# Kernel optimization log

Measured on AMD Instinct MI355X. Metric: run time of the kernel, lower is better.

The kernel has to match this reference:

```python
import jax, jax.numpy as jnp
import numpy as np
import math

N_HEAD = 12

def alibi_slopes(h):
    x = (2 ** 8) ** (1.0 / h)
    return jnp.array([1.0 / x ** (i + 1) for i in range(h)], dtype=jnp.float32)

def setup_inputs() -> dict:
    key = jax.random.key(0)
    k0, k1, k2 = jax.random.split(key, 3)
    B, T, C = 4, 2048, 576
    x = jax.random.normal(k0, (B, T, C), dtype=jnp.float32)
    w_qkv = jax.random.normal(k1, (3 * C, C), dtype=jnp.float32) * 0.02
    w_proj = jax.random.normal(k2, (C, C), dtype=jnp.float32) * 0.02
    return {"x": x, "w_qkv": w_qkv, "w_proj": w_proj}

def reference(x, w_qkv, w_proj):
    B, T, C = x.shape
    H = N_HEAD
    D = C // H
    qkv = x @ w_qkv.T  # [B,T,3C]
    q, k, v = jnp.split(qkv, 3, axis=2)
    q = q.reshape(B, T, H, D).transpose(0, 2, 1, 3)  # [B,H,T,D]
    k = k.reshape(B, T, H, D).transpose(0, 2, 1, 3)
    v = v.reshape(B, T, H, D).transpose(0, 2, 1, 3)
    # value residual with v1=None: v = 0.5*v + 0.5*v = v (faithful no-op)
    scale = 1.0 / math.sqrt(D)
    att = jnp.einsum('bhid,bhjd->bhij', q, k) * scale  # [B,H,T,T]
    # ALiBi bias as written: (col - row).clamp(min=0) * slope (zero on causal part)
    col = jnp.arange(T, dtype=jnp.float32)[None, :]
    row = jnp.arange(T, dtype=jnp.float32)[:, None]
    bias = jnp.maximum(col - row, 0.0)[None, :, :] * alibi_slopes(H)[:, None, None]  # [H,T,T]
    att = att + bias[None]
    causal = (jnp.arange(T)[None, :] <= jnp.arange(T)[:, None])  # [T,T] lower-tri
    att = jnp.where(causal[None, None], att, -jnp.inf)
    att = jax.nn.softmax(att, axis=-1)
    y = jnp.einsum('bhij,bhjd->bhid', att, v)  # [B,H,T,D]
    y = y.transpose(0, 2, 1, 3).reshape(B, T, C)
    return y @ w_proj.T
```

## Files before the change

### kernel.cpp

```cpp
#include <hip/hip_runtime.h>
#include <math.h>

#define Bn 4
#define Tn 2048
#define Cn 576
#define Hn 12
#define Dn 48
#define Mn (Bn*Tn)

#define QSCALE (1.4426950408889634f * 0.14433756729740643f)

typedef short  short8  __attribute__((ext_vector_type(8)));
typedef float  floatx4 __attribute__((ext_vector_type(4)));
typedef unsigned short ushort_t;
typedef unsigned short ushort8_t __attribute__((ext_vector_type(8)));

static __device__ __forceinline__ unsigned short f2bf(float f) {
    union { float f; unsigned int u; } v; v.f = f;
    unsigned int r = v.u + 0x7FFFu + ((v.u >> 16) & 1u);
    return (unsigned short)(r >> 16);
}

static __device__ __forceinline__ unsigned int pack_trunc(float a, float b) {
    union { float f; unsigned int u; } ua, ub; ua.f = a; ub.f = b;
    return (ua.u >> 16) | (ub.u & 0xFFFF0000u);
}

static __device__ __forceinline__ void gload16(void* lds, const void* g) {
    __builtin_amdgcn_global_load_lds(
        (const __attribute__((address_space(1))) void*)g,
        (__attribute__((address_space(3))) void*)lds, 16, 0, 0);
}

__global__ __launch_bounds__(256)
void cast3(const float* __restrict__ a, ushort_t* __restrict__ oa, int na4,
           const float* __restrict__ b, ushort_t* __restrict__ ob, int nb4,
           const float* __restrict__ c, ushort_t* __restrict__ oc, int nc4)
{
    int i = blockIdx.x * 256 + threadIdx.x;
    const float* src; ushort_t* dst; int idx;
    if (i < na4)                  { src = a; dst = oa; idx = i; }
    else if (i < na4 + nb4)       { src = b; dst = ob; idx = i - na4; }
    else if (i < na4 + nb4 + nc4) { src = c; dst = oc; idx = i - na4 - nb4; }
    else return;
    float4 v = ((const float4*)src)[idx];
    ushort4 o;
    o.x = f2bf(v.x); o.y = f2bf(v.y); o.z = f2bf(v.z); o.w = f2bf(v.w);
    ((ushort4*)dst)[idx] = o;
}

template<int MODE, int MTILE>
__global__ __launch_bounds__(256)
void gemm_mfma(const ushort_t* __restrict__ A, const ushort_t* __restrict__ W,
               ushort_t* __restrict__ outb, float* __restrict__ outf)
{
    constexpr int SA   = MTILE / 16;
    constexpr int NSEG = SA + 4;
    constexpr int PW   = NSEG / 4;
    constexpr int MF   = MTILE / 64;
    constexpr int NB   = (MODE == 0) ? 27 : 9;
    __shared__ __align__(16) ushort_t Ls[2][NSEG][512];

    const int tid  = threadIdx.x;
    const int wave = tid >> 6;
    const int lane = tid & 63;
    const int m    = lane & 15;
    const int g    = lane >> 4;
    const int bid  = blockIdx.x;
    const int xcd  = bid & 7;
    const int slot = bid >> 3;
    const int n0   = (slot % NB) * 64;
    const int m0   = (xcd + 8 * (slot / NB)) * MTILE;

    floatx4 acc[MF][4];
    #pragma unroll
    for (int i = 0; i < MF; ++i)
        #pragma unroll
        for (int j = 0; j < 4; ++j)
            acc[i][j] = (floatx4){0.f, 0.f, 0.f, 0.f};

    const char* gp[PW];
    int         si[PW];
    #pragma unroll
    for (int i = 0; i < PW; ++i) {
        int s = wave + i * 4;
        si[i] = s;
        gp[i] = (s < SA)
            ? (const char*)(A + (size_t)(m0 + s * 16 + m) * Cn + g * 8)
            : (const char*)(W + (size_t)(n0 + (s - SA) * 16 + m) * Cn + g * 8);
    }

    #pragma unroll
    for (int i = 0; i < PW; ++i) { gload16(&Ls[0][si[i]][0], gp[i]); gp[i] += 64; }
    __syncthreads();

    int buf = 0;
    for (int k0 = 0; k0 < Cn; k0 += 32) {
        if (k0 + 32 < Cn) {
            #pragma unroll
            for (int i = 0; i < PW; ++i) { gload16(&Ls[buf ^ 1][si[i]][0], gp[i]); gp[i] += 64; }
        }
        short8 bf4[4];
        #pragma unroll
        for (int j = 0; j < 4; ++j) bf4[j] = *(const short8*)&Ls[buf][SA + j][lane * 8];
        #pragma unroll
        for (int i = 0; i < MF; ++i) {
            short8 af = *(const short8*)&Ls[buf][wave * MF + i][lane * 8];
            #pragma unroll
            for (int j = 0; j < 4; ++j)
                acc[i][j] = __builtin_amdgcn_mfma_f32_16x16x32_bf16(af, bf4[j], acc[i][j], 0, 0, 0);
        }
        __syncthreads();
        buf ^= 1;
    }

    const size_t per = (size_t)Bn * Hn * Tn * Dn;
    if (MODE == 0) {
        const int which = n0 / Cn;
        const int nb    = n0 - which * Cn;
        const int b     = m0 >> 11;
        const int t0g   = m0 & 2047;
        ushort_t* Lc = (ushort_t*)&Ls[0][0][0];
        if (which == 2) {
            constexpr int RS = MTILE + 8;
            #pragma unroll
            for (int i = 0; i < MF; ++i)
                #pragma unroll
                for (int j = 0; j < 4; ++j) {
                    ushort4 pk;
                    pk.x = f2bf(acc[i][j][0]); pk.y = f2bf(acc[i][j][1]);
                    pk.z = f2bf(acc[i][j][2]); pk.w = f2bf(acc[i][j][3]);
                    *(ushort4*)&Lc[(j * 16 + m) * RS + wave * (MTILE / 4) + i * 16 + g * 4] = pk;
                }
            __syncthreads();
            constexpr int CPC = MTILE / 8;
            constexpr int NIT = 64 * CPC / 256;
            #pragma unroll
            for (int it = 0; it < NIT; ++it) {
                int c    = tid + it * 256;
                int col  = c / CPC;
                int rowc = (c - col * CPC) * 8;
                int n    = nb + col;
                int h    = n / 48;
                int d    = n - h * 48;
                ushort_t* dst = outb + 2 * per
                    + (((size_t)(b * Hn + h) * Dn + d) * Tn) + t0g + rowc;
                *(ushort8_t*)dst = *(const ushort8_t*)&Lc[col * RS + rowc];
            }
        } else {
            const float sc = (which == 0) ? QSCALE : 1.0f;
            #pragma unroll
            for (int i = 0; i < MF; ++i)
                #pragma unroll
                for (int j = 0; j < 4; ++j)
                    #pragma unroll
                    for (int r = 0; r < 4; ++r)
                        Lc[(wave * (MTILE / 4) + i * 16 + g * 4 + r) * 80 + j * 16 + m] =
                            f2bf(acc[i][j][r] * sc);
            __syncthreads();
            constexpr int NIT = MTILE * 8 / 256;
            #pragma unroll
            for (int it = 0; it < NIT; ++it) {
                int c   = tid + it * 256;
                int row = c >> 3;
                int c8  = (c & 7) * 8;
                int n   = nb + c8;
                int h   = n / 48;
                int d   = n - h * 48;
                ushort_t* dst = outb + (size_t)which * per
                    + (((size_t)(b * Hn + h) * Tn + t0g + row) * Dn) + d;
                *(ushort8_t*)dst = *(const ushort8_t*)&Lc[row * 80 + c8];
            }
        }
    } else {
        #pragma unroll
        for (int i = 0; i < MF; ++i) {
            #pragma unroll
            for (int r = 0; r < 4; ++r) {
                int mrow = m0 + wave * (MTILE / 4) + i * 16 + g * 4 + r;
                #pragma unroll
                for (int j = 0; j < 4; ++j)
                    outf[(size_t)mrow * Cn + n0 + j * 16 + m] = acc[i][j][r];
            }
        }
    }
}

__global__ __launch_bounds__(512, 6)
void attn_mfma(const ushort_t* __restrict__ Q, const ushort_t* __restrict__ K,
               const ushort_t* __restrict__ V, ushort_t* __restrict__ Y,
               const ushort_t* __restrict__ zb)
{
    __shared__ __align__(16) ushort_t QPs[16][512];
    __shared__ __align__(16) ushort_t Ks[2][8][512];
    __shared__ __align__(16) ushort_t Vs[2][6][512];

    const int id   = blockIdx.x;
    const int kk   = id / 48;
    const int bh   = id - kk * 48;
    const int QT   = (kk & 1) ? (kk >> 1) : (15 - (kk >> 1));
    const int tid  = threadIdx.x;
    const int wave = tid >> 6;
    const int lane = tid & 63;
    const int m    = lane & 15;
    const int g    = lane >> 4;
    const int q0   = QT * 128;
    const int nkt  = 2 * QT + 2;

    const ushort_t* Qp = Q + (size_t)bh * Tn * Dn;
    const ushort_t* Kp = K + (size_t)bh * Tn * Dn;
    const ushort_t* Vp = V + (size_t)bh * Dn * Tn;

    {
        const char* qrp = (const char*)(Qp + (size_t)(q0 + wave * 16 + m) * Dn);
        gload16(&QPs[wave * 2 + 0][0], qrp + g * 16);
        gload16(&QPs[wave * 2 + 1][0], (g < 2) ? (qrp + 64 + g * 16) : (const char*)zb);
    }

    const bool  kpad = ((wave & 1) == 1) && (g >= 2);
    const char* kptr = kpad ? (const char*)zb
        : (const char*)(Kp + (size_t)((wave >> 1) * 16 + m) * Dn) + (wave & 1) * 64 + g * 16;
    const int   kadv = kpad ? 0 : 64 * Dn * 2;
    const char* vptr = (const char*)(Vp + (size_t)((wave >> 1) * 16 + m) * Tn)
                       + (wave & 1) * 64 + g * 16;
    const int   vadv = 64 * 2;

    gload16(&Ks[0][wave][0], kptr); kptr += kadv;
    if (wave < 6) { gload16(&Vs[0][wave][0], vptr); vptr += vadv; }
    __syncthreads();

    short8 bq[2];
    bq[0] = *(const short8*)&QPs[wave * 2 + 0][lane * 8];
    bq[1] = *(const short8*)&QPs[wave * 2 + 1][lane * 8];

    floatx4 acc[3];
    #pragma unroll
    for (int t = 0; t < 3; ++t) acc[t] = (floatx4){0.f, 0.f, 0.f, 0.f};
    float l_tot = 0.f;
    const int qrow  = q0 + wave * 16 + m;
    const int qwmin = q0 + wave * 16;
    const int qwmax = qwmin + 15;

    for (int jt = 0; jt < nkt; ++jt) {
        const int cur = jt & 1;
        const int j0  = jt * 64;
        if (jt + 1 < nkt) {
            gload16(&Ks[cur ^ 1][wave][0], kptr); kptr += kadv;
            if (wave < 6) { gload16(&Vs[cur ^ 1][wave][0], vptr); vptr += vadv; }
        }

        if (j0 <= qwmax) {
            floatx4 s[4];
            #pragma unroll
            for (int t = 0; t < 4; ++t) {
                s[t] = (floatx4){0.f, 0.f, 0.f, 0.f};
                #pragma unroll
                for (int kc = 0; kc < 2; ++kc) {
                    short8 ak = *(const short8*)&Ks[cur][t * 2 + kc][lane * 8];
                    s[t] = __builtin_amdgcn_mfma_f32_16x16x32_bf16(ak, bq[kc], s[t], 0, 0, 0);
                }
            }

            float p[4][4];
            float lsum = 0.f;
            if (j0 + 63 > qwmin) {
                #pragma unroll
                for (int t = 0; t < 4; ++t)
                    #pragma unroll
                    for (int r = 0; r < 4; ++r) {
                        int j = j0 + t * 16 + g * 4 + r;
                        float v = (j <= qrow) ? s[t][r] : -1e30f;
                        float e = __builtin_amdgcn_exp2f(v);
                        p[t][r] = e; lsum += e;
                    }
            } else {
                #pragma unroll
                for (int t = 0; t < 4; ++t)
                    #pragma unroll
                    for (int r = 0; r < 4; ++r) {
                        float e = __builtin_amdgcn_exp2f(s[t][r]);
                        p[t][r] = e; lsum += e;
                    }
            }
            lsum += __shfl_xor(lsum, 16);
            lsum += __shfl_xor(lsum, 32);
            l_tot += lsum;

            #pragma unroll
            for (int t = 0; t < 4; ++t) {
                uint2 w2;
                w2.x = pack_trunc(p[t][0], p[t][1]);
                w2.y = pack_trunc(p[t][2], p[t][3]);
                *(uint2*)&QPs[wave * 2 + (t >> 1)]
                             [(2 * (t & 1) + (g >> 1)) * 128 + m * 8 + (g & 1) * 4] = w2;
            }
            asm volatile("s_waitcnt lgkmcnt(0)" ::: "memory");

            #pragma unroll
            for (int kc = 0; kc < 2; ++kc) {
                short8 bp = *(const short8*)&QPs[wave * 2 + kc][lane * 8];
                #pragma unroll
                for (int t = 0; t < 3; ++t) {
                    short8 av = *(const short8*)&Vs[cur][t * 2 + kc][lane * 8];
                    acc[t] = __builtin_amdgcn_mfma_f32_16x16x32_bf16(av, bp, acc[t], 0, 0, 0);
                }
            }
        }

        __syncthreads();
    }

    const float inv = 1.0f / l_tot;
    const int b = bh / Hn;
    const int h = bh - b * Hn;
    ushort_t* yp = Y + ((size_t)(b * Tn + qrow)) * Cn + h * Dn;
    #pragma unroll
    for (int t = 0; t < 3; ++t) {
        ushort4 o;
        o.x = f2bf(acc[t][0] * inv);
        o.y = f2bf(acc[t][1] * inv);
        o.z = f2bf(acc[t][2] * inv);
        o.w = f2bf(acc[t][3] * inv);
        *(ushort4*)&yp[t * 16 + g * 4] = o;
    }
}

extern "C" void kernel_launch(void* const* d_in, const int* in_sizes, int n_in,
                              void* d_out, int out_size, void* d_ws, size_t ws_size,
                              hipStream_t stream)
{
    const float* x      = (const float*)d_in[0];
    const float* w_qkv  = (const float*)d_in[1];
    const float* w_proj = (const float*)d_in[2];
    float* out = (float*)d_out;

    const size_t per = (size_t)Bn * Hn * Tn * Dn;

    ushort_t* xb  = (ushort_t*)d_ws;
    ushort_t* wqb = xb  + (size_t)Mn * Cn;
    ushort_t* wpb = wqb + (size_t)3 * Cn * Cn;
    ushort_t* qkv = wpb + (size_t)Cn * Cn;
    ushort_t* yb  = qkv + 3 * per;
    ushort_t* zb  = yb  + (size_t)Mn * Cn;

    hipMemsetAsync(zb, 0, 256, stream);

    const int na4 = Mn * Cn / 4, nb4 = 3 * Cn * Cn / 4, nc4 = Cn * Cn / 4;
    cast3<<<dim3((na4 + nb4 + nc4 + 255) / 256), dim3(256), 0, stream>>>(
        x, xb, na4, w_qkv, wqb, nb4, w_proj, wpb, nc4);

    gemm_mfma<0, 256><<<dim3((Mn / 256) * 27), dim3(256), 0, stream>>>(xb, wqb, qkv, nullptr);

    attn_mfma<<<dim3((Tn / 128) * Bn * Hn), dim3(512), 0, stream>>>(
        qkv, qkv + per, qkv + 2 * per, yb, zb);

    gemm_mfma<1, 128><<<dim3((Mn / 128) * 9), dim3(256), 0, stream>>>(yb, wpb, nullptr, out);
}
```

Baseline: 186.5 us.

## Load GEMM operands directly into registers instead of staging through LDS

```diff
diff --git a/kernel.cpp b/kernel.cpp
--- a/kernel.cpp
+++ b/kernel.cpp
@@ -49,17 +49,14 @@
     ((ushort4*)dst)[idx] = o;
 }
 
-template<int MODE, int MTILE>
-__global__ __launch_bounds__(256)
+template<int MODE>
+__global__ __launch_bounds__(256, 2)
 void gemm_mfma(const ushort_t* __restrict__ A, const ushort_t* __restrict__ W,
                ushort_t* __restrict__ outb, float* __restrict__ outf)
 {
-    constexpr int SA   = MTILE / 16;
-    constexpr int NSEG = SA + 4;
-    constexpr int PW   = NSEG / 4;
-    constexpr int MF   = MTILE / 64;
-    constexpr int NB   = (MODE == 0) ? 27 : 9;
-    __shared__ __align__(16) ushort_t Ls[2][NSEG][512];
+    constexpr int NB    = (MODE == 0) ? 27 : 9;
+    constexpr int NSTEP = Cn / 32;
+    __shared__ __align__(16) ushort_t Ep[4][64 * 72];
 
     const int tid  = threadIdx.x;
     const int wave = tid >> 6;
@@ -70,114 +67,106 @@
     const int xcd  = bid & 7;
     const int slot = bid >> 3;
     const int n0   = (slot % NB) * 64;
-    const int m0   = (xcd + 8 * (slot / NB)) * MTILE;
-
-    floatx4 acc[MF][4];
-    #pragma unroll
-    for (int i = 0; i < MF; ++i)
+    const int m0   = (xcd + 8 * (slot / NB)) * 256;
+    const int mw   = m0 + wave * 64;
+
+    const ushort_t* pa[4];
+    const ushort_t* pb[4];
+    #pragma unroll
+    for (int i = 0; i < 4; ++i) {
+        pa[i] = A + (size_t)(mw + i * 16 + m) * Cn + g * 8;
+        pb[i] = W + (size_t)(n0 + i * 16 + m) * Cn + g * 8;
+    }
+
+    floatx4 acc[4][4];
+    #pragma unroll
+    for (int i = 0; i < 4; ++i)
         #pragma unroll
         for (int j = 0; j < 4; ++j)
             acc[i][j] = (floatx4){0.f, 0.f, 0.f, 0.f};
 
-    const char* gp[PW];
-    int         si[PW];
-    #pragma unroll
-    for (int i = 0; i < PW; ++i) {
-        int s = wave + i * 4;
-        si[i] = s;
-        gp[i] = (s < SA)
-            ? (const char*)(A + (size_t)(m0 + s * 16 + m) * Cn + g * 8)
-            : (const char*)(W + (size_t)(n0 + (s - SA) * 16 + m) * Cn + g * 8);
-    }
-
-    #pragma unroll
-    for (int i = 0; i < PW; ++i) { gload16(&Ls[0][si[i]][0], gp[i]); gp[i] += 64; }
-    __syncthreads();
-
-    int buf = 0;
-    for (int k0 = 0; k0 < Cn; k0 += 32) {
-        if (k0 + 32 < Cn) {
-            #pragma unroll
-            for (int i = 0; i < PW; ++i) { gload16(&Ls[buf ^ 1][si[i]][0], gp[i]); gp[i] += 64; }
-        }
-        short8 bf4[4];
+    short8 fa[2][4], fb[2][4];
+    #pragma unroll
+    for (int i = 0; i < 4; ++i) { fa[0][i] = *(const short8*)pa[i];
+                                  fb[0][i] = *(const short8*)pb[i]; }
+
+    #pragma unroll
+    for (int k = 0; k < NSTEP; ++k) {
+        const int c = k & 1;
+        if (k + 1 < NSTEP) {
+            #pragma unroll
+            for (int i = 0; i < 4; ++i) {
+                fa[c ^ 1][i] = *(const short8*)(pa[i] + (k + 1) * 32);
+                fb[c ^ 1][i] = *(const short8*)(pb[i] + (k + 1) * 32);
+            }
+        }
         #pragma unroll
-        for (int j = 0; j < 4; ++j) bf4[j] = *(const short8*)&Ls[buf][SA + j][lane * 8];
-        #pragma unroll
-        for (int i = 0; i < MF; ++i) {
-            short8 af = *(const short8*)&Ls[buf][wave * MF + i][lane * 8];
+        for (int i = 0; i < 4; ++i)
             #pragma unroll
             for (int j = 0; j < 4; ++j)
-                acc[i][j] = __builtin_amdgcn_mfma_f32_16x16x32_bf16(af, bf4[j], acc[i][j], 0, 0, 0);
-        }
-        __syncthreads();
-        buf ^= 1;
+                acc[i][j] = __builtin_amdgcn_mfma_f32_16x16x32_bf16(fa[c][i], fb[c][j], acc[i][j], 0, 0, 0);
     }
 
     const size_t per = (size_t)Bn * Hn * Tn * Dn;
     if (MODE == 0) {
         const int which = n0 / Cn;
         const int nb    = n0 - which * Cn;
-        const int b     = m0 >> 11;
-        const int t0g   = m0 & 2047;
-        ushort_t* Lc = (ushort_t*)&Ls[0][0][0];
+        const int b     = mw >> 11;
+        const int t0w   = mw & 2047;
+        ushort_t* Lw = &Ep[wave][0];
         if (which == 2) {
-            constexpr int RS = MTILE + 8;
-            #pragma unroll
-            for (int i = 0; i < MF; ++i)
+            #pragma unroll
+            for (int i = 0; i < 4; ++i)
                 #pragma unroll
                 for (int j = 0; j < 4; ++j) {
                     ushort4 pk;
                     pk.x = f2bf(acc[i][j][0]); pk.y = f2bf(acc[i][j][1]);
                     pk.z = f2bf(acc[i][j][2]); pk.w = f2bf(acc[i][j][3]);
-                    *(ushort4*)&Lc[(j * 16 + m) * RS + wave * (MTILE / 4) + i * 16 + g * 4] = pk;
+                    *(ushort4*)&Lw[(j * 16 + m) * 72 + i * 16 + g * 4] = pk;
                 }
-            __syncthreads();
-            constexpr int CPC = MTILE / 8;
-            constexpr int NIT = 64 * CPC / 256;
-            #pragma unroll
-            for (int it = 0; it < NIT; ++it) {
-                int c    = tid + it * 256;
-                int col  = c / CPC;
-                int rowc = (c - col * CPC) * 8;
+            asm volatile("s_waitcnt lgkmcnt(0)" ::: "memory");
+            #pragma unroll
+            for (int it = 0; it < 8; ++it) {
+                int c    = it * 64 + lane;
+                int col  = c >> 3;
+                int rowc = (c & 7) * 8;
                 int n    = nb + col;
                 int h    = n / 48;
                 int d    = n - h * 48;
                 ushort_t* dst = outb + 2 * per
-                    + (((size_t)(b * Hn + h) * Dn + d) * Tn) + t0g + rowc;
-                *(ushort8_t*)dst = *(const ushort8_t*)&Lc[col * RS + rowc];
+                    + (((size_t)(b * Hn + h) * Dn + d) * Tn) + t0w + rowc;
+                *(ushort8_t*)dst = *(const ushort8_t*)&Lw[col * 72 + rowc];
             }
         } else {
             const float sc = (which == 0) ? QSCALE : 1.0f;
             #pragma unroll
-            for (int i = 0; i < MF; ++i)
+            for (int i = 0; i < 4; ++i)
                 #pragma unroll
                 for (int j = 0; j < 4; ++j)
                     #pragma unroll
                     for (int r = 0; r < 4; ++r)
-                        Lc[(wave * (MTILE / 4) + i * 16 + g * 4 + r) * 80 + j * 16 + m] =
+                        Lw[(i * 16 + g * 4 + r) * 72 + j * 16 + m] =
                             f2bf(acc[i][j][r] * sc);
-            __syncthreads();
-            constexpr int NIT = MTILE * 8 / 256;
-            #pragma unroll
-            for (int it = 0; it < NIT; ++it) {
-                int c   = tid + it * 256;
+            asm volatile("s_waitcnt lgkmcnt(0)" ::: "memory");
+            #pragma unroll
+            for (int it = 0; it < 8; ++it) {
+                int c   = it * 64 + lane;
                 int row = c >> 3;
                 int c8  = (c & 7) * 8;
                 int n   = nb + c8;
                 int h   = n / 48;
                 int d   = n - h * 48;
                 ushort_t* dst = outb + (size_t)which * per
-                    + (((size_t)(b * Hn + h) * Tn + t0g + row) * Dn) + d;
-                *(ushort8_t*)dst = *(const ushort8_t*)&Lc[row * 80 + c8];
+                    + (((size_t)(b * Hn + h) * Tn + t0w + row) * Dn) + d;
+                *(ushort8_t*)dst = *(const ushort8_t*)&Lw[row * 72 + c8];
             }
         }
     } else {
         #pragma unroll
-        for (int i = 0; i < MF; ++i) {
+        for (int i = 0; i < 4; ++i) {
             #pragma unroll
             for (int r = 0; r < 4; ++r) {
-                int mrow = m0 + wave * (MTILE / 4) + i * 16 + g * 4 + r;
+                int mrow = mw + i * 16 + g * 4 + r;
                 #pragma unroll
                 for (int j = 0; j < 4; ++j)
                     outf[(size_t)mrow * Cn + n0 + j * 16 + m] = acc[i][j][r];
@@ -349,10 +338,10 @@
     cast3<<<dim3((na4 + nb4 + nc4 + 255) / 256), dim3(256), 0, stream>>>(
         x, xb, na4, w_qkv, wqb, nb4, w_proj, wpb, nc4);
 
-    gemm_mfma<0, 256><<<dim3((Mn / 256) * 27), dim3(256), 0, stream>>>(xb, wqb, qkv, nullptr);
+    gemm_mfma<0><<<dim3((Mn / 256) * 27), dim3(256), 0, stream>>>(xb, wqb, qkv, nullptr);
 
     attn_mfma<<<dim3((Tn / 128) * Bn * Hn), dim3(512), 0, stream>>>(
         qkv, qkv + per, qkv + 2 * per, yb, zb);
 
-    gemm_mfma<1, 128><<<dim3((Mn / 128) * 9), dim3(256), 0, stream>>>(yb, wpb, nullptr, out);
-}
+    gemm_mfma<1><<<dim3((Mn / 256) * 9), dim3(256), 0, stream>>>(yb, wpb, nullptr, out);
+}
```

Result: slower. 219.5 us (+17.7%).
